# Kernel optimization log

Measured on AMD Instinct MI355X. Metric: run time of the kernel, lower is better.

## Reference

```python
import jax, jax.numpy as jnp
import numpy as np

EPS = 1e-5

def layer_norm(x, g, b):
    mu = jnp.mean(x, axis=-1, keepdims=True)
    var = jnp.var(x, axis=-1, keepdims=True)
    return (x - mu) * jax.lax.rsqrt(var + EPS) * g + b

def setup_inputs() -> dict:
    key = jax.random.key(0)
    ks = jax.random.split(key, 12)
    B, N, D, H = 32, 577, 768, 12
    Dh = D // H
    hid = 4 * D
    s = lambda d: 1.0 / np.sqrt(d)
    return {
        "x": jax.random.normal(ks[0], (B, N, D), jnp.float32),
        "ln1_g": jnp.ones((D,), jnp.float32),
        "ln1_b": jnp.zeros((D,), jnp.float32),
        "ln2_g": jnp.ones((D,), jnp.float32),
        "ln2_b": jnp.zeros((D,), jnp.float32),
        "w_qkv": jax.random.normal(ks[1], (D, 3 * D), jnp.float32) * s(D),
        "b_qkv": jnp.zeros((3 * D,), jnp.float32),
        "w_proj": jax.random.normal(ks[2], (D, D), jnp.float32) * s(D),
        "b_proj": jnp.zeros((D,), jnp.float32),
        "w_fc1": jax.random.normal(ks[3], (D, hid), jnp.float32) * s(D),
        "b_fc1": jnp.zeros((hid,), jnp.float32),
        "w_fc2": jax.random.normal(ks[4], (hid, D), jnp.float32) * s(hid),
        "b_fc2": jnp.zeros((D,), jnp.float32),
    }

def reference(x, ln1_g, ln1_b, ln2_g, ln2_b, w_qkv, b_qkv, w_proj, b_proj,
              w_fc1, b_fc1, w_fc2, b_fc2):
    B, N, D = x.shape
    H = 12
    Dh = D // H
    scale = Dh ** -0.5
    # --- attention branch ---
    h = layer_norm(x, ln1_g, ln1_b)
    qkv = h @ w_qkv + b_qkv                      # [B, N, 3D]
    qkv = qkv.reshape(B, N, 3, H, Dh).transpose(2, 0, 3, 1, 4)  # [3, B, H, N, Dh]
    q, k, v = qkv[0], qkv[1], qkv[2]
    attn = jnp.einsum('bhnd,bhmd->bhnm', q, k) * scale  # [B, H, N, N]
    attn = jax.nn.softmax(attn, axis=-1)
    o = jnp.einsum('bhnm,bhmd->bhnd', attn, v)           # [B, H, N, Dh]
    o = o.transpose(0, 2, 1, 3).reshape(B, N, D)
    o = o @ w_proj + b_proj
    x = x + o
    # --- MLP branch ---
    h = layer_norm(x, ln2_g, ln2_b)
    h = jnp.clip(h @ w_fc1 + b_fc1, 0.0, 6.0)            # ReLU6
    h = h @ w_fc2 + b_fc2
    return x + h
```

## Files before the change

### kernel.cpp

```cpp
#include <hip/hip_runtime.h>
#include <math.h>


typedef unsigned short u16;
typedef _Float16 f16;
typedef __attribute__((ext_vector_type(8))) _Float16 f16x8;
typedef __attribute__((ext_vector_type(4))) float f32x4;

__device__ __forceinline__ u16 f2h(float x) {
    union { f16 h; u16 u; } cv;
    cv.h = (f16)x;
    return cv.u;
}
__device__ __forceinline__ float h2f(u16 b) {
    union { u16 u; f16 h; } cv;
    cv.u = b;
    return (float)cv.h;
}
__device__ __forceinline__ void load_lds16(const u16* g, void* l) {
    __builtin_amdgcn_global_load_lds(
        (const __attribute__((address_space(1))) void*)g,
        (__attribute__((address_space(3))) void*)l, 16, 0, 0);
}
__device__ __forceinline__ int xcd_swz(int lid, int nwg) {
    const int x = lid & 7, pos = lid >> 3;
    const int q = nwg >> 3, r = nwg & 7;
    return (x < r ? x * (q + 1) : r * (q + 1) + (x - r) * q) + pos;
}

__global__ __launch_bounds__(256)
void wprep_kernel(const float* __restrict__ W, u16* __restrict__ Th,
                  int K, int N)
{
    __shared__ float t[32][33];
    const int n0 = blockIdx.x * 32, k0 = blockIdx.y * 32;
    const int tr = threadIdx.x >> 3, tc4 = (threadIdx.x & 7) * 4;
    const float4 v = *(const float4*)&W[(size_t)(k0 + tr) * N + n0 + tc4];
    t[tr][tc4 + 0] = v.x; t[tr][tc4 + 1] = v.y;
    t[tr][tc4 + 2] = v.z; t[tr][tc4 + 3] = v.w;
    __syncthreads();
    ushort4 h;
    h.x = f2h(t[tc4 + 0][tr]);
    h.y = f2h(t[tc4 + 1][tr]);
    h.z = f2h(t[tc4 + 2][tr]);
    h.w = f2h(t[tc4 + 3][tr]);
    *(ushort4*)&Th[(size_t)(n0 + tr) * K + k0 + tc4] = h;
}

__global__ __launch_bounds__(256)
void ln_kernel(const float* __restrict__ x, const float* __restrict__ g,
               const float* __restrict__ beta, u16* __restrict__ oh)
{
    const int row = blockIdx.x;
    const int tid = threadIdx.x;
    const float* xr = x + (size_t)row * 768;
    const float v0 = xr[tid], v1 = xr[tid + 256], v2 = xr[tid + 512];
    float s  = v0 + v1 + v2;
    float ss = v0 * v0 + v1 * v1 + v2 * v2;
    #pragma unroll
    for (int off = 1; off < 64; off <<= 1) {
        s  += __shfl_xor(s, off);
        ss += __shfl_xor(ss, off);
    }
    __shared__ float redS[4], redQ[4];
    const int wid = tid >> 6;
    if ((tid & 63) == 0) { redS[wid] = s; redQ[wid] = ss; }
    __syncthreads();
    s  = redS[0] + redS[1] + redS[2] + redS[3];
    ss = redQ[0] + redQ[1] + redQ[2] + redQ[3];
    const float mean = s * (1.0f / 768.0f);
    const float var  = ss * (1.0f / 768.0f) - mean * mean;
    const float rstd = rsqrtf(var + 1e-5f);
    u16* ohr = oh + (size_t)row * 768;
    #pragma unroll
    for (int u = 0; u < 3; ++u) {
        const int c = tid + u * 256;
        const float vv = (u == 0) ? v0 : (u == 1) ? v1 : v2;
        ohr[c] = f2h((vv - mean) * rstd * g[c] + beta[c]);
    }
}

template<int RELU6, int RES, int OMODE>
__global__ __launch_bounds__(256)
void mfma_gemm(const u16* __restrict__ Ah, const u16* __restrict__ Bh,
               const float* __restrict__ bias, const float* res,
               float* Cf, u16* __restrict__ Ch,
               u16* __restrict__ Qh_, u16* __restrict__ Kh_,
               u16* __restrict__ Vth_,
               int M, int N, int K)
{
    __shared__ u16 lds[32768];

    const int tid  = threadIdx.x;
    const int wave = tid >> 6;
    const int lane = tid & 63;

    const int nwg = gridDim.x * gridDim.y;
    int lid = blockIdx.y * gridDim.x + blockIdx.x;
    lid = xcd_swz(lid, nwg);
    const int bm = (lid / gridDim.x) * 128;
    const int bn = (lid % gridDim.x) * 128;

    const int rl = lane >> 2;
    const int c  = lane & 3;
    const int r0 = wave * 16 + rl;
    const int r1 = 64 + r0;
    const int kgA0 = (((r0 >> 3) & 1) << 2) | (c ^ ((r0 >> 1) & 3));
    const int kgA1 = (((r1 >> 3) & 1) << 2) | (c ^ ((r1 >> 1) & 3));

    const u16* pA00 = Ah + (size_t)(bm + r0) * K + kgA0 * 8;
    const u16* pA01 = Ah + (size_t)(bm + r0) * K + (kgA0 ^ 4) * 8;
    const u16* pA10 = Ah + (size_t)(bm + r1) * K + kgA1 * 8;
    const u16* pA11 = Ah + (size_t)(bm + r1) * K + (kgA1 ^ 4) * 8;
    const u16* pB00 = Bh + (size_t)(bn + r0) * K + kgA0 * 8;
    const u16* pB01 = Bh + (size_t)(bn + r0) * K + (kgA0 ^ 4) * 8;
    const u16* pB10 = Bh + (size_t)(bn + r1) * K + kgA1 * 8;
    const u16* pB11 = Bh + (size_t)(bn + r1) * K + (kgA1 ^ 4) * 8;

    char* ldsb = (char*)lds;
    char* dA00 = ldsb +     0 + wave * 1024;
    char* dA01 = ldsb +  8192 + wave * 1024;
    char* dA10 = ldsb +  4096 + wave * 1024;
    char* dA11 = ldsb + 12288 + wave * 1024;
    char* dB00 = ldsb + 16384 + wave * 1024;
    char* dB01 = ldsb + 24576 + wave * 1024;
    char* dB10 = ldsb + 20480 + wave * 1024;
    char* dB11 = ldsb + 28672 + wave * 1024;

    const int am0 = (wave >> 1) * 64;
    const int bn0 = (wave & 1) * 64;
    const int l15 = lane & 15;
    const int lg  = lane >> 4;

    f32x4 acc[4][4] = {};
    const int np = K >> 6;

    load_lds16(pA00, dA00); load_lds16(pA01, dA01);
    load_lds16(pA10, dA10); load_lds16(pA11, dA11);
    load_lds16(pB00, dB00); load_lds16(pB01, dB01);
    load_lds16(pB10, dB10); load_lds16(pB11, dB11);
    pA00 += 64; pA01 += 64; pA10 += 64; pA11 += 64;
    pB00 += 64; pB01 += 64; pB10 += 64; pB11 += 64;

    int cur = 0;
    for (int p = 0; p < np; ++p) {
        asm volatile("s_waitcnt vmcnt(0)" ::: "memory");
        __builtin_amdgcn_s_barrier();
        if (p + 1 < np) {
            const int o = (cur ^ 1) << 15;
            load_lds16(pA00, dA00 + o); load_lds16(pA01, dA01 + o);
            load_lds16(pA10, dA10 + o); load_lds16(pA11, dA11 + o);
            load_lds16(pB00, dB00 + o); load_lds16(pB01, dB01 + o);
            load_lds16(pB10, dB10 + o); load_lds16(pB11, dB11 + o);
            pA00 += 64; pA01 += 64; pA10 += 64; pA11 += 64;
            pB00 += 64; pB01 += 64; pB10 += 64; pB11 += 64;
        }
        const u16* sA = lds + (cur << 14);
        const u16* sB = sA + 8192;

        #pragma unroll
        for (int ss = 0; ss < 2; ++ss) {
            f16x8 ah[4];
            #pragma unroll
            for (int fm = 0; fm < 4; ++fm) {
                const int ar = am0 + fm * 16 + l15;
                const int kg = ss * 4 + lg;
                const int pc = (kg & 3) ^ ((ar >> 1) & 3);
                const int pt = (kg >> 2) ^ ((ar >> 3) & 1);
                ah[fm] = *(const f16x8*)&sA[pt * 4096 + ar * 32 + pc * 8];
            }
            #pragma unroll
            for (int fn = 0; fn < 4; ++fn) {
                const int br = bn0 + fn * 16 + l15;
                const int kg = ss * 4 + lg;
                const int pc = (kg & 3) ^ ((br >> 1) & 3);
                const int pt = (kg >> 2) ^ ((br >> 3) & 1);
                const f16x8 bh = *(const f16x8*)&sB[pt * 4096 + br * 32 + pc * 8];
                #pragma unroll
                for (int fm = 0; fm < 4; ++fm)
                    acc[fm][fn] = __builtin_amdgcn_mfma_f32_16x16x32_f16(
                        ah[fm], bh, acc[fm][fn], 0, 0, 0);
            }
        }
        cur ^= 1;
    }

    if (OMODE == 2) {
        __syncthreads();
        const int s  = bn / 768;
        const int hh = ((bn + bn0) - s * 768) >> 6;
        u16* eph = lds + wave * 4352;
        #pragma unroll
        for (int fn = 0; fn < 4; ++fn) {
            const float bv = bias[bn + bn0 + fn * 16 + l15];
            #pragma unroll
            for (int fm = 0; fm < 4; ++fm) {
                const f32x4 v = acc[fm][fn];
                #pragma unroll
                for (int j = 0; j < 4; ++j) {
                    const float o = v[j] + bv;
                    const int idx = (s == 2)
                        ? (fn * 16 + l15) * 68 + fm * 16 + lg * 4 + j
                        : (fm * 16 + lg * 4 + j) * 68 + fn * 16 + l15;
                    eph[idx] = f2h(o);
                }
            }
        }
        __syncthreads();
        if (s == 2) {
            const int r = bm + am0 + lane;
            const bool ok = r < M;
            const int b = (unsigned)r / 577u;
            const int n = r - b * 577;
            u16* dh = Vth_ + (size_t)(b * 12 + hh) * 64 * 640 + n;
            #pragma unroll 8
            for (int d = 0; d < 64; ++d) {
                const u16 vh = eph[d * 68 + lane];
                if (ok) dh[(size_t)d * 640] = vh;
            }
        } else {
            u16* base = (s == 0) ? Qh_ : Kh_;
            #pragma unroll 8
            for (int rr = 0; rr < 64; ++rr) {
                const int r = bm + am0 + rr;
                if (r < M) {
                    const int b = (unsigned)r / 577u;
                    const int n = r - b * 577;
                    base[((size_t)((b * 12 + hh) * 577 + n)) * 64 + lane] =
                        eph[rr * 68 + lane];
                }
            }
        }
    } else {
        #pragma unroll
        for (int fn = 0; fn < 4; ++fn) {
            const int cc = bn + bn0 + fn * 16 + l15;
            const float bv = bias[cc];
            #pragma unroll
            for (int fm = 0; fm < 4; ++fm) {
                const int rbase = bm + am0 + fm * 16 + lg * 4;
                const f32x4 v = acc[fm][fn];
                #pragma unroll
                for (int j = 0; j < 4; ++j) {
                    const int r = rbase + j;
                    if (r < M) {
                        float o = v[j] + bv;
                        if (RELU6) o = fminf(fmaxf(o, 0.0f), 6.0f);
                        if (RES)   o += res[(size_t)r * N + cc];
                        if (OMODE == 0) Cf[(size_t)r * N + cc] = o;
                        else            Ch[(size_t)r * N + cc] = f2h(o);
                    }
                }
            }
        }
    }
}

__global__ __launch_bounds__(256)
void attn_mfma(const u16* __restrict__ Qh, const u16* __restrict__ Kh,
               const u16* __restrict__ Vth, u16* __restrict__ Oh)
{
    constexpr int SEQ = 577, NP = 640;
    __shared__ u16 sK[2 * 4096], sV[2 * 4096];
    __shared__ u16 sPh[4][16 * 72];

    const int tid  = threadIdx.x;
    const int wave = tid >> 6;
    const int lane = tid & 63;
    const int l15 = lane & 15, lg = lane >> 4;

    const int nwg = gridDim.x * gridDim.y;
    int lid = blockIdx.y * gridDim.x + blockIdx.x;
    lid = xcd_swz(lid, nwg);
    const int q0 = (lid % gridDim.x) * 64;
    const int bh = lid / gridDim.x;

    const size_t qkBase = (size_t)bh * SEQ * 64;
    const size_t vBase  = (size_t)bh * 64 * NP;

    f16x8 qfh[2];
    {
        const size_t ro = qkBase + (size_t)(q0 + wave * 16 + l15) * 64;
        #pragma unroll
        for (int ks = 0; ks < 2; ++ks)
            qfh[ks] = *(const f16x8*)&Qh[ro + (ks * 4 + lg) * 8];
    }

    const int srow = lane >> 3;
    const int sc   = lane & 7;

    f32x4 oacc[4] = {};
    float mrun = -1e30f, lrun = 0.0f;
    constexpr int NT = 10;

    #pragma unroll
    for (int t = 0; t < 2; ++t) {
        const int row = wave * 16 + t * 8 + srow;
        const int lc  = sc ^ (row & 7);
        load_lds16(Kh + qkBase + (size_t)row * 64 + lc * 8,
                   (char*)sK + wave * 2048 + t * 1024);
        load_lds16(Vth + vBase + (size_t)row * NP + lc * 8,
                   (char*)sV + wave * 2048 + t * 1024);
    }
    __syncthreads();

    int cur = 0;
    for (int it = 0; it < NT; ++it) {
        const int kv0 = it * 64;
        if (it + 1 < NT) {
            const int nkv = kv0 + 64;
            const int o = (cur ^ 1) * 8192;
            #pragma unroll
            for (int t = 0; t < 2; ++t) {
                const int row = wave * 16 + t * 8 + srow;
                const int lc  = sc ^ (row & 7);
                load_lds16(Kh + qkBase + (size_t)(nkv + row) * 64 + lc * 8,
                           (char*)sK + o + wave * 2048 + t * 1024);
                load_lds16(Vth + vBase + (size_t)row * NP + nkv + lc * 8,
                           (char*)sV + o + wave * 2048 + t * 1024);
            }
        }
        const u16* sKc = sK + cur * 4096;
        const u16* sVc = sV + cur * 4096;

        f32x4 sacc[4] = {};
        __builtin_amdgcn_s_setprio(1);
        #pragma unroll
        for (int fkv = 0; fkv < 4; ++fkv) {
            const int row = fkv * 16 + l15;
            #pragma unroll
            for (int ks = 0; ks < 2; ++ks) {
                const int ph = ((ks * 4 + lg) ^ (row & 7)) * 8;
                const f16x8 kh = *(const f16x8*)&sKc[row * 64 + ph];
                sacc[fkv] = __builtin_amdgcn_mfma_f32_16x16x32_f16(
                    kh, qfh[ks], sacc[fkv], 0, 0, 0);
            }
        }
        __builtin_amdgcn_s_setprio(0);

        float p[4][4];
        float mt = -1e30f;
        const bool tail = (kv0 + 64 > SEQ);
        #pragma unroll
        for (int fkv = 0; fkv < 4; ++fkv)
            #pragma unroll
            for (int j = 0; j < 4; ++j) {
                float sv = sacc[fkv][j] * 0.125f;
                if (tail && (kv0 + fkv * 16 + lg * 4 + j >= SEQ)) sv = -1e30f;
                p[fkv][j] = sv;
                mt = fmaxf(mt, sv);
            }
        mt = fmaxf(mt, __shfl_xor(mt, 16));
        mt = fmaxf(mt, __shfl_xor(mt, 32));
        const float mnew = fmaxf(mrun, mt);
        const float corr = __expf(mrun - mnew);
        float rs = 0.0f;
        #pragma unroll
        for (int fkv = 0; fkv < 4; ++fkv)
            #pragma unroll
            for (int j = 0; j < 4; ++j) {
                p[fkv][j] = __expf(p[fkv][j] - mnew);
                rs += p[fkv][j];
            }
        rs += __shfl_xor(rs, 16);
        rs += __shfl_xor(rs, 32);
        lrun = lrun * corr + rs;
        mrun = mnew;
        #pragma unroll
        for (int fd = 0; fd < 4; ++fd)
            #pragma unroll
            for (int j = 0; j < 4; ++j) oacc[fd][j] *= corr;

        u16* phr = &sPh[wave][l15 * 72];
        #pragma unroll
        for (int fkv = 0; fkv < 4; ++fkv) {
            ushort4 hv;
            hv.x = f2h(p[fkv][0]);
            hv.y = f2h(p[fkv][1]);
            hv.z = f2h(p[fkv][2]);
            hv.w = f2h(p[fkv][3]);
            *(ushort4*)&phr[fkv * 16 + lg * 4] = hv;
        }

        __builtin_amdgcn_s_setprio(1);
        #pragma unroll
        for (int ks = 0; ks < 2; ++ks) {
            const f16x8 pbh = *(const f16x8*)&sPh[wave][l15 * 72 + (ks * 4 + lg) * 8];
            #pragma unroll
            for (int fd = 0; fd < 4; ++fd) {
                const int row = fd * 16 + l15;
                const int ph = ((ks * 4 + lg) ^ (row & 7)) * 8;
                const f16x8 vh = *(const f16x8*)&sVc[row * 64 + ph];
                oacc[fd] = __builtin_amdgcn_mfma_f32_16x16x32_f16(
                    vh, pbh, oacc[fd], 0, 0, 0);
            }
        }
        __builtin_amdgcn_s_setprio(0);

        __syncthreads();
        cur ^= 1;
    }

    const int q = q0 + wave * 16 + l15;
    if (q < SEQ) {
        const float inv = 1.0f / lrun;
        const int b = bh / 12, h = bh % 12;
        const size_t rowo = ((size_t)b * SEQ + q) * 768 + h * 64;
        #pragma unroll
        for (int fd = 0; fd < 4; ++fd) {
            ushort4 hv;
            hv.x = f2h(oacc[fd][0] * inv);
            hv.y = f2h(oacc[fd][1] * inv);
            hv.z = f2h(oacc[fd][2] * inv);
            hv.w = f2h(oacc[fd][3] * inv);
            *(ushort4*)&Oh[rowo + fd * 16 + lg * 4] = hv;
        }
    }
}

extern "C" void kernel_launch(void* const* d_in, const int* in_sizes, int n_in,
                              void* d_out, int out_size, void* d_ws, size_t ws_size,
                              hipStream_t stream)
{
    const float* x      = (const float*)d_in[0];
    const float* ln1_g  = (const float*)d_in[1];
    const float* ln1_b  = (const float*)d_in[2];
    const float* ln2_g  = (const float*)d_in[3];
    const float* ln2_b  = (const float*)d_in[4];
    const float* w_qkv  = (const float*)d_in[5];
    const float* b_qkv  = (const float*)d_in[6];
    const float* w_proj = (const float*)d_in[7];
    const float* b_proj = (const float*)d_in[8];
    const float* w_fc1  = (const float*)d_in[9];
    const float* b_fc1  = (const float*)d_in[10];
    const float* w_fc2  = (const float*)d_in[11];
    const float* b_fc2  = (const float*)d_in[12];
    float* out = (float*)d_out;

    const int M  = 18464;
    const int Mp = 18560;

    char* p = (char*)d_ws;
    u16* Wqkv  = (u16*)p;    p += (size_t)2304 * 768 * 2;
    u16* Wproj = (u16*)p;    p += (size_t)768 * 768 * 2;
    u16* Wfc1  = (u16*)p;    p += (size_t)3072 * 768 * 2;
    u16* Wfc2  = (u16*)p;    p += (size_t)768 * 3072 * 2;
    u16* A_h = (u16*)p;      p += (size_t)Mp * 768 * 2;
    const size_t QKB = ((size_t)384 * 577 * 64 + 8192) * 2;
    u16* Qh = (u16*)p;       p += QKB;
    u16* Kh = (u16*)p;       p += QKB;
    u16* Vth = (u16*)p;      p += (size_t)384 * 64 * 640 * 2;
    u16* fc1h = (u16*)p;     p += (size_t)Mp * 3072 * 2;

    wprep_kernel<<<dim3(72, 24),  256, 0, stream>>>(w_qkv,  Wqkv,  768, 2304);
    wprep_kernel<<<dim3(24, 24),  256, 0, stream>>>(w_proj, Wproj, 768, 768);
    wprep_kernel<<<dim3(96, 24),  256, 0, stream>>>(w_fc1,  Wfc1,  768, 3072);
    wprep_kernel<<<dim3(24, 96),  256, 0, stream>>>(w_fc2,  Wfc2,  3072, 768);

    ln_kernel<<<M, 256, 0, stream>>>(x, ln1_g, ln1_b, A_h);
    mfma_gemm<0, 0, 2><<<dim3(18, 145), 256, 0, stream>>>(
        A_h, Wqkv, b_qkv, nullptr, nullptr, nullptr,
        Qh, Kh, Vth, M, 2304, 768);
    attn_mfma<<<dim3(10, 384), 256, 0, stream>>>(Qh, Kh, Vth, A_h);
    mfma_gemm<0, 1, 0><<<dim3(6, 145), 256, 0, stream>>>(
        A_h, Wproj, b_proj, x, out, nullptr,
        nullptr, nullptr, nullptr, M, 768, 768);
    ln_kernel<<<M, 256, 0, stream>>>(out, ln2_g, ln2_b, A_h);
    mfma_gemm<1, 0, 1><<<dim3(24, 145), 256, 0, stream>>>(
        A_h, Wfc1, b_fc1, nullptr, nullptr, fc1h,
        nullptr, nullptr, nullptr, M, 3072, 768);
    mfma_gemm<0, 1, 0><<<dim3(6, 145), 256, 0, stream>>>(
        fc1h, Wfc2, b_fc2, out, out, nullptr,
        nullptr, nullptr, nullptr, M, 768, 3072);
}
```

Measured before the change: 616.9 us.

## Pad sequence to 640 per batch and chunk MLP to reuse workspace

```diff
diff --git a/kernel.cpp b/kernel.cpp
--- a/kernel.cpp
+++ b/kernel.cpp
@@ -49,7 +49,7 @@
 
 __global__ __launch_bounds__(256)
 void ln_kernel(const float* __restrict__ x, const float* __restrict__ g,
-               const float* __restrict__ beta, u16* __restrict__ oh)
+               const float* __restrict__ beta, u16* __restrict__ oh, int pad)
 {
     const int row = blockIdx.x;
     const int tid = threadIdx.x;
@@ -71,7 +71,12 @@
     const float mean = s * (1.0f / 768.0f);
     const float var  = ss * (1.0f / 768.0f) - mean * mean;
     const float rstd = rsqrtf(var + 1e-5f);
-    u16* ohr = oh + (size_t)row * 768;
+    int row_p = row;
+    if (pad) {
+        const unsigned bb = (unsigned)row / 577u;
+        row_p = (int)(bb * 640u + ((unsigned)row - bb * 577u));
+    }
+    u16* ohr = oh + (size_t)row_p * 768;
     #pragma unroll
     for (int u = 0; u < 3; ++u) {
         const int c = tid + u * 256;
@@ -80,7 +85,7 @@
     }
 }
 
-template<int RELU6, int RES, int OMODE>
+template<int RELU6, int RES, int OMODE, int PADMAP>
 __global__ __launch_bounds__(256)
 void mfma_gemm(const u16* __restrict__ Ah, const u16* __restrict__ Bh,
                const float* __restrict__ bias, const float* res,
@@ -189,6 +194,9 @@
         __syncthreads();
         const int s  = bn / 768;
         const int hh = ((bn + bn0) - s * 768) >> 6;
+        const int gr0 = bm + am0;
+        const int bb  = gr0 / 640;
+        const int n0  = gr0 - bb * 640;
         u16* eph = lds + wave * 4352;
         #pragma unroll
         for (int fn = 0; fn < 4; ++fn) {
@@ -208,28 +216,16 @@
         }
         __syncthreads();
         if (s == 2) {
-            const int r = bm + am0 + lane;
-            const bool ok = r < M;
-            const int b = (unsigned)r / 577u;
-            const int n = r - b * 577;
-            u16* dh = Vth_ + (size_t)(b * 12 + hh) * 64 * 640 + n;
+            u16* dh = Vth_ + (size_t)(bb * 12 + hh) * 64 * 640 + n0 + lane;
             #pragma unroll 8
-            for (int d = 0; d < 64; ++d) {
-                const u16 vh = eph[d * 68 + lane];
-                if (ok) dh[(size_t)d * 640] = vh;
-            }
+            for (int d = 0; d < 64; ++d)
+                dh[(size_t)d * 640] = eph[d * 68 + lane];
         } else {
-            u16* base = (s == 0) ? Qh_ : Kh_;
+            u16* base = ((s == 0) ? Qh_ : Kh_) +
+                        ((size_t)(bb * 12 + hh) * 640 + n0) * 64 + lane;
             #pragma unroll 8
-            for (int rr = 0; rr < 64; ++rr) {
-                const int r = bm + am0 + rr;
-                if (r < M) {
-                    const int b = (unsigned)r / 577u;
-                    const int n = r - b * 577;
-                    base[((size_t)((b * 12 + hh) * 577 + n)) * 64 + lane] =
-                        eph[rr * 68 + lane];
-                }
-            }
+            for (int rr = 0; rr < 64; ++rr)
+                base[(size_t)rr * 64] = eph[rr * 68 + lane];
         }
     } else {
         #pragma unroll
@@ -243,7 +239,17 @@
                 #pragma unroll
                 for (int j = 0; j < 4; ++j) {
                     const int r = rbase + j;
-                    if (r < M) {
+                    if (PADMAP) {
+                        const int bb = r / 640;
+                        const int nn = r - bb * 640;
+                        if (nn < 577) {
+                            const size_t ro = (size_t)(bb * 577 + nn) * N + cc;
+                            float o = v[j] + bv;
+                            if (RELU6) o = fminf(fmaxf(o, 0.0f), 6.0f);
+                            if (RES)   o += res[ro];
+                            Cf[ro] = o;
+                        }
+                    } else if (r < M) {
                         float o = v[j] + bv;
                         if (RELU6) o = fminf(fmaxf(o, 0.0f), 6.0f);
                         if (RES)   o += res[(size_t)r * N + cc];
@@ -275,7 +281,7 @@
     const int q0 = (lid % gridDim.x) * 64;
     const int bh = lid / gridDim.x;
 
-    const size_t qkBase = (size_t)bh * SEQ * 64;
+    const size_t qkBase = (size_t)bh * NP * 64;
     const size_t vBase  = (size_t)bh * 64 * NP;
 
     f16x8 qfh[2];
@@ -405,7 +411,7 @@
     if (q < SEQ) {
         const float inv = 1.0f / lrun;
         const int b = bh / 12, h = bh % 12;
-        const size_t rowo = ((size_t)b * SEQ + q) * 768 + h * 64;
+        const size_t rowo = ((size_t)(b * 640 + q)) * 768 + h * 64;
         #pragma unroll
         for (int fd = 0; fd < 4; ++fd) {
             ushort4 hv;
@@ -438,38 +444,42 @@
     float* out = (float*)d_out;
 
     const int M  = 18464;
-    const int Mp = 18560;
+    const int Mq = 20480;
 
     char* p = (char*)d_ws;
     u16* Wqkv  = (u16*)p;    p += (size_t)2304 * 768 * 2;
     u16* Wproj = (u16*)p;    p += (size_t)768 * 768 * 2;
     u16* Wfc1  = (u16*)p;    p += (size_t)3072 * 768 * 2;
     u16* Wfc2  = (u16*)p;    p += (size_t)768 * 3072 * 2;
-    u16* A_h = (u16*)p;      p += (size_t)Mp * 768 * 2;
-    const size_t QKB = ((size_t)384 * 577 * 64 + 8192) * 2;
-    u16* Qh = (u16*)p;       p += QKB;
-    u16* Kh = (u16*)p;       p += QKB;
+    u16* A_h = (u16*)p;      p += (size_t)Mq * 768 * 2;
+    u16* Qh  = (u16*)p;      p += (size_t)384 * 640 * 64 * 2;
+    u16* Kh  = (u16*)p;      p += (size_t)384 * 640 * 64 * 2;
     u16* Vth = (u16*)p;      p += (size_t)384 * 64 * 640 * 2;
-    u16* fc1h = (u16*)p;     p += (size_t)Mp * 3072 * 2;
+    u16* fc1h = Qh;
 
     wprep_kernel<<<dim3(72, 24),  256, 0, stream>>>(w_qkv,  Wqkv,  768, 2304);
     wprep_kernel<<<dim3(24, 24),  256, 0, stream>>>(w_proj, Wproj, 768, 768);
     wprep_kernel<<<dim3(96, 24),  256, 0, stream>>>(w_fc1,  Wfc1,  768, 3072);
     wprep_kernel<<<dim3(24, 96),  256, 0, stream>>>(w_fc2,  Wfc2,  3072, 768);
 
-    ln_kernel<<<M, 256, 0, stream>>>(x, ln1_g, ln1_b, A_h);
-    mfma_gemm<0, 0, 2><<<dim3(18, 145), 256, 0, stream>>>(
+    ln_kernel<<<M, 256, 0, stream>>>(x, ln1_g, ln1_b, A_h, 1);
+    mfma_gemm<0, 0, 2, 0><<<dim3(18, 160), 256, 0, stream>>>(
         A_h, Wqkv, b_qkv, nullptr, nullptr, nullptr,
-        Qh, Kh, Vth, M, 2304, 768);
+        Qh, Kh, Vth, Mq, 2304, 768);
     attn_mfma<<<dim3(10, 384), 256, 0, stream>>>(Qh, Kh, Vth, A_h);
-    mfma_gemm<0, 1, 0><<<dim3(6, 145), 256, 0, stream>>>(
+    mfma_gemm<0, 1, 0, 1><<<dim3(6, 160), 256, 0, stream>>>(
         A_h, Wproj, b_proj, x, out, nullptr,
-        nullptr, nullptr, nullptr, M, 768, 768);
-    ln_kernel<<<M, 256, 0, stream>>>(out, ln2_g, ln2_b, A_h);
-    mfma_gemm<1, 0, 1><<<dim3(24, 145), 256, 0, stream>>>(
-        A_h, Wfc1, b_fc1, nullptr, nullptr, fc1h,
-        nullptr, nullptr, nullptr, M, 3072, 768);
-    mfma_gemm<0, 1, 0><<<dim3(6, 145), 256, 0, stream>>>(
-        fc1h, Wfc2, b_fc2, out, out, nullptr,
-        nullptr, nullptr, nullptr, M, 768, 3072);
-}
+        nullptr, nullptr, nullptr, Mq, 768, 768);
+    ln_kernel<<<M, 256, 0, stream>>>(out, ln2_g, ln2_b, A_h, 0);
+    const int CH = 9344;
+    for (int r0 = 0; r0 < M; r0 += CH) {
+        const int mc = (M - r0 < CH) ? (M - r0) : CH;
+        const int mtiles = (mc + 127) / 128;
+        mfma_gemm<1, 0, 1, 0><<<dim3(24, mtiles), 256, 0, stream>>>(
+            A_h + (size_t)r0 * 768, Wfc1, b_fc1, nullptr, nullptr, fc1h,
+            nullptr, nullptr, nullptr, mc, 3072, 768);
+        mfma_gemm<0, 1, 0, 0><<<dim3(6, mtiles), 256, 0, stream>>>(
+            fc1h, Wfc2, b_fc2, out + (size_t)r0 * 768, out + (size_t)r0 * 768,
+            nullptr, nullptr, nullptr, nullptr, mc, 768, 3072);
+    }
+}
```

New measurement: 624.2 us. Within noise of the previous version (+1.2%).
